# Kernel optimization log

Measured on AMD Instinct MI355X. Metric: run time of the kernel, lower is better.

Reference implementation:

```python
import jax, jax.numpy as jnp
import numpy as np


def _ln(x, g, b, eps=1e-5):
    m = x.mean(-1, keepdims=True)
    v = ((x - m) ** 2).mean(-1, keepdims=True)
    return g * (x - m) / jnp.sqrt(v + eps) + b


def _mha(x, w_qkv, b_qkv, w_o, b_o, nh):
    B, S, d = x.shape
    hd = d // nh
    qkv = x @ w_qkv.T + b_qkv
    q, k, v = jnp.split(qkv, 3, axis=-1)
    sp = lambda t: t.reshape(B, S, nh, hd).transpose(0, 2, 1, 3)
    q, k, v = sp(q), sp(k), sp(v)
    a = jax.nn.softmax(jnp.einsum('bhqd,bhkd->bhqk', q, k) / np.float32(np.sqrt(hd)), axis=-1)
    o = jnp.einsum('bhqk,bhkd->bhqd', a, v).transpose(0, 2, 1, 3).reshape(B, S, d)
    return o @ w_o.T + b_o


def _enc(x, w_qkv, b_qkv, w_o, b_o, ga, ba, wf1, bf1, wf2, bf2, gb, bb, nh=2):
    # torch TransformerEncoderLayer, post-norm, ReLU FFN
    x = _ln(x + _mha(x, w_qkv, b_qkv, w_o, b_o, nh), ga, ba)
    ff = jax.nn.relu(x @ wf1.T + bf1) @ wf2.T + bf2
    return _ln(x + ff, gb, bb)


def forward(nodes, w_qkv1, b_qkv1, w_o1, b_o1, g1a, bb1a, w_ff1a, bf1a, w_ff1b, bf1b, g1b, bb1b,
            wq, bq, wk, bk, wv, bv, g_co, bb_co, w4, b4, w5, b5, w6, b6,
            w_rel, w_root, b_rgcn, wg_rel, wg_root, bg,
            w_qkv2, b_qkv2, w_o2, b_o2, g2a, bb2a, w_ff2a, bf2a, w_ff2b, bf2b, g2b, bb2b,
            w_l1, b_l1, w_l2, b_l2, edge_index, opt_idx):
    N, H = nodes.shape
    O = 4
    B = opt_idx.shape[0] // O
    # option-node mutual attention (encoder_layer1) + scatter back
    opts = nodes[opt_idx].reshape(B, O, H)
    opts = _enc(opts, w_qkv1, b_qkv1, w_o1, b_o1, g1a, bb1a, w_ff1a, bf1a, w_ff1b, bf1b, g1b, bb1b)
    nodes2 = nodes.at[opt_idx].set(opts.reshape(B * O, H))
    src, dst = edge_index[0], edge_index[1]
    xs, xd = nodes2[src], nodes2[dst]  # [E,H]
    # per-edge 4-head co-attention: node1/node2 are single rows so qk^T is a scalar per head
    hd = H // 4
    q = (xs @ wq.T + bq).reshape(-1, 4, hd)
    k = (xd @ wk.T + bk).reshape(-1, 4, hd)
    v = (xd @ wv.T + bv).reshape(-1, 4, hd)
    s = jnp.einsum('ehd,ehd->eh', q, k) / np.float32(np.sqrt(hd))
    r = (s[..., None] * v).reshape(-1, H)
    co = jax.nn.relu(_ln(r, g_co, bb_co))
    h = jax.nn.relu(co @ w4.T + b4)
    h = jax.nn.relu(h @ w5.T + b5)
    logits = h @ w6.T + b6  # [E,8]
    # original applies Softmax(dim=0) to a [1,8] tensor -> all ones -> argmax picks class 0
    probs = jax.nn.softmax(logits[:, None, :], axis=1)[:, 0, :]
    edge_type = jnp.argmax(probs, axis=-1)
    # RGCNConv(H, H, num_relations=8), mean aggregation per relation + root + bias
    agg = jnp.zeros((N, H), nodes.dtype)
    for rel in range(8):
        m = edge_type == rel
        msg = jnp.where(m[:, None], xs @ w_rel[rel], 0.0)
        ssum = jax.ops.segment_sum(msg, dst, num_segments=N)
        cnt = jax.ops.segment_sum(m.astype(nodes.dtype), dst, num_segments=N)
        agg = agg + ssum / jnp.maximum(cnt, 1.0)[:, None]
    out1 = nodes2 @ w_root + b_rgcn + agg
    # GraphConv(H, 64): add-aggregated neighbors through lin_rel + root through lin_root
    agg2 = jax.ops.segment_sum(out1[src], dst, num_segments=N)
    out2 = agg2 @ wg_rel + bg + out1 @ wg_root  # [N,64]
    # readout over option nodes (encoder_layer2 + tanh(linear1) + linear2)
    opt2 = out2[opt_idx].reshape(B, O, 64)
    opt2 = _enc(opt2, w_qkv2, b_qkv2, w_o2, b_o2, g2a, bb2a, w_ff2a, bf2a, w_ff2b, bf2b, g2b, bb2b)
    opt2 = jnp.tanh(opt2 @ w_l1.T + b_l1)
    return opt2 @ w_l2.T + b_l2  # [B,O,1]


def setup_inputs() -> dict:
    key = jax.random.key(0)
    N, E, B, O, H, F = 20000, 40000, 64, 4, 768, 2048
    ks = iter(jax.random.split(key, 64))
    W = lambda *s: jax.random.normal(next(ks), s, jnp.float32) * 0.02
    return dict(
        nodes=jax.random.normal(next(ks), (N, H), jnp.float32),
        edge_index=jax.random.randint(next(ks), (2, E), 0, N),
        opt_idx=jnp.arange(B * O),
        w_qkv1=W(3 * H, H), b_qkv1=jnp.zeros(3 * H), w_o1=W(H, H), b_o1=jnp.zeros(H),
        g1a=jnp.ones(H), bb1a=jnp.zeros(H),
        w_ff1a=W(F, H), bf1a=jnp.zeros(F), w_ff1b=W(H, F), bf1b=jnp.zeros(H),
        g1b=jnp.ones(H), bb1b=jnp.zeros(H),
        wq=W(H, H), bq=jnp.zeros(H), wk=W(H, H), bk=jnp.zeros(H), wv=W(H, H), bv=jnp.zeros(H),
        g_co=jnp.ones(H), bb_co=jnp.zeros(H),
        w4=W(H, H), b4=jnp.zeros(H), w5=W(64, H), b5=jnp.zeros(64), w6=W(8, 64), b6=jnp.zeros(8),
        w_rel=W(8, H, H), w_root=W(H, H), b_rgcn=jnp.zeros(H),
        wg_rel=W(H, 64), wg_root=W(H, 64), bg=jnp.zeros(64),
        w_qkv2=W(192, 64), b_qkv2=jnp.zeros(192), w_o2=W(64, 64), b_o2=jnp.zeros(64),
        g2a=jnp.ones(64), bb2a=jnp.zeros(64),
        w_ff2a=W(F, 64), bf2a=jnp.zeros(F), w_ff2b=W(64, F), bf2b=jnp.zeros(64),
        g2b=jnp.ones(64), bb2b=jnp.zeros(64),
        w_l1=W(64, 64), b_l1=jnp.zeros(64), w_l2=W(1, 64), b_l2=jnp.zeros(1),
    )


def reference(nodes, edge_index, opt_idx, w_qkv1, b_qkv1, w_o1, b_o1, g1a, bb1a, w_ff1a, bf1a,
              w_ff1b, bf1b, g1b, bb1b, wq, bq, wk, bk, wv, bv, g_co, bb_co, w4, b4, w5, b5, w6, b6,
              w_rel, w_root, b_rgcn, wg_rel, wg_root, bg, w_qkv2, b_qkv2, w_o2, b_o2, g2a, bb2a,
              w_ff2a, bf2a, w_ff2b, bf2b, g2b, bb2b, w_l1, b_l1, w_l2, b_l2):
    return forward(nodes, w_qkv1, b_qkv1, w_o1, b_o1, g1a, bb1a, w_ff1a, bf1a, w_ff1b, bf1b, g1b,
                   bb1b, wq, bq, wk, bk, wv, bv, g_co, bb_co, w4, b4, w5, b5, w6, b6, w_rel, w_root,
                   b_rgcn, wg_rel, wg_root, bg, w_qkv2, b_qkv2, w_o2, b_o2, g2a, bb2a, w_ff2a, bf2a,
                   w_ff2b, bf2b, g2b, bb2b, w_l1, b_l1, w_l2, b_l2, edge_index, opt_idx)
```

## Files before the change

### kernel.cpp

```cpp
#include <hip/hip_runtime.h>

typedef unsigned short u16;
typedef unsigned int u32;
typedef __bf16 bf16x8 __attribute__((ext_vector_type(8)));
typedef float f32x4 __attribute__((ext_vector_type(4)));

__device__ __forceinline__ u16 f2bf(float f) {
    union { float f; u32 u; } v; v.f = f;
    u32 r = v.u + 0x7FFFu + ((v.u >> 16) & 1u);
    return (u16)(r >> 16);
}
__device__ __forceinline__ float bf2f(u16 h) {
    union { u32 u; float f; } v; v.u = (u32)h << 16; return v.f;
}

__global__ __launch_bounds__(256) void gemm_bt(
    const u16* __restrict__ A, const u16* __restrict__ Bt,
    float* __restrict__ C, u16* __restrict__ Cb, const float* __restrict__ bias,
    int M, int N, int K, int relu)
{
    __shared__ char lA[128 * 64 * 2];
    __shared__ char lB[128 * 64 * 2];
    const int t = threadIdx.x;
    const int w = t >> 6, l = t & 63;
    const int bn = blockIdx.x, bm = blockIdx.y;
    const int wr = w >> 1, wc = w & 1;

    const int srow = w * 8 + (l >> 3);
    const int scol = ((l & 7) ^ (l >> 3)) << 3;
    const u16* gA = A + (size_t)(bm * 128 + srow) * K + scol;
    const u16* gB = Bt + (size_t)(bn * 128 + srow) * K + scol;

    f32x4 zero = {0.f, 0.f, 0.f, 0.f};
    f32x4 acc[4][4];
#pragma unroll
    for (int i = 0; i < 4; i++)
#pragma unroll
        for (int j = 0; j < 4; j++) acc[i][j] = zero;

    const int arow = wr * 64 + (l & 15);
    const int brow = wc * 64 + (l & 15);
    const int kx = l >> 4;
    const int sw = l & 7;

    for (int k0 = 0; k0 < K; k0 += 64) {
#pragma unroll
        for (int c2 = 0; c2 < 4; ++c2) {
            __builtin_amdgcn_global_load_lds(
                (const __attribute__((address_space(1))) void*)(gA + (size_t)c2 * 32 * K + k0),
                (__attribute__((address_space(3))) void*)(lA + c2 * 4096 + w * 1024), 16, 0, 0);
            __builtin_amdgcn_global_load_lds(
                (const __attribute__((address_space(1))) void*)(gB + (size_t)c2 * 32 * K + k0),
                (__attribute__((address_space(3))) void*)(lB + c2 * 4096 + w * 1024), 16, 0, 0);
        }
        __syncthreads();
#pragma unroll
        for (int kk = 0; kk < 2; ++kk) {
            bf16x8 af[4], bfr[4];
#pragma unroll
            for (int mi = 0; mi < 4; ++mi)
                af[mi] = *(const bf16x8*)(lA + (arow + mi * 16) * 128 + (((kk * 4 + kx) ^ sw) << 4));
#pragma unroll
            for (int ni = 0; ni < 4; ++ni)
                bfr[ni] = *(const bf16x8*)(lB + (brow + ni * 16) * 128 + (((kk * 4 + kx) ^ sw) << 4));
#pragma unroll
            for (int mi = 0; mi < 4; ++mi)
#pragma unroll
                for (int ni = 0; ni < 4; ++ni)
                    acc[mi][ni] = __builtin_amdgcn_mfma_f32_16x16x32_bf16(af[mi], bfr[ni], acc[mi][ni], 0, 0, 0);
        }
        __syncthreads();
    }

    const int cm = bm * 128 + wr * 64;
    const int cn = bn * 128 + wc * 64;
#pragma unroll
    for (int mi = 0; mi < 4; ++mi) {
#pragma unroll
        for (int ni = 0; ni < 4; ++ni) {
            int row0 = cm + mi * 16 + (l >> 4) * 4;
            int col = cn + ni * 16 + (l & 15);
            float bv = bias ? bias[col] : 0.f;
#pragma unroll
            for (int r = 0; r < 4; ++r) {
                float v = acc[mi][ni][r] + bv;
                if (relu) v = fmaxf(v, 0.f);
                if (Cb) Cb[(size_t)(row0 + r) * N + col] = f2bf(v);
                else    C [(size_t)(row0 + r) * N + col] = v;
            }
        }
    }
}

struct CJob { const float* src; u16* dst; long n4; };
struct CJobs4 { CJob j[4]; };
__global__ void conv4_bf16(CJobs4 jobs)
{
    CJob jb = jobs.j[blockIdx.z];
    long i = (long)blockIdx.x * blockDim.x + threadIdx.x;
    long stride = (long)gridDim.x * blockDim.x;
    for (; i < jb.n4; i += stride) {
        float4 v = ((const float4*)jb.src)[i];
        ushort4 o;
        o.x = f2bf(v.x); o.y = f2bf(v.y); o.z = f2bf(v.z); o.w = f2bf(v.w);
        ((ushort4*)jb.dst)[i] = o;
    }
}

struct TJob { const float* src; u16* dst; int Rr, Cc, ldo; };
struct TJobs4 { TJob j[4]; };
__global__ void transpose4_bf16(TJobs4 jobs)
{
    TJob jb = jobs.j[blockIdx.z];
    __shared__ float tile[32][33];
    int c0 = blockIdx.x * 32, r0 = blockIdx.y * 32;
    if (c0 >= jb.Cc || r0 >= jb.Rr) return;
    int tx = threadIdx.x, ty = threadIdx.y;
    for (int dy = 0; dy < 32; dy += 8) {
        int r = r0 + ty + dy, c = c0 + tx;
        tile[ty + dy][tx] = (r < jb.Rr && c < jb.Cc) ? jb.src[(size_t)r * jb.Cc + c] : 0.f;
    }
    __syncthreads();
    for (int dy = 0; dy < 32; dy += 8) {
        int c = c0 + ty + dy, r = r0 + tx;
        if (c < jb.Cc && r < jb.Rr) jb.dst[(size_t)c * jb.ldo + r] = f2bf(tile[tx][ty + dy]);
    }
}

__global__ void conv_nodes_str(const float* __restrict__ nodes, u16* __restrict__ Abig,
                               int Nn, int Mpad)
{
    long i = (long)blockIdx.x * blockDim.x + threadIdx.x;
    long stride = (long)gridDim.x * blockDim.x;
    long n4 = (long)Mpad * 192;
    for (; i < n4; i += stride) {
        long row = i / 192, c4 = i % 192;
        ushort4 o;
        if ((int)row < Nn) {
            float4 v = ((const float4*)nodes)[i];
            o.x = f2bf(v.x); o.y = f2bf(v.y); o.z = f2bf(v.z); o.w = f2bf(v.w);
        } else { o.x = 0; o.y = 0; o.z = 0; o.w = 0; }
        ((ushort4*)Abig)[row * 384 + c4] = o;
    }
}

__global__ void gather_x0(const float* __restrict__ nodes, const int* __restrict__ opt,
                          float* __restrict__ x0, u16* __restrict__ x0b, int H)
{
    int r = blockIdx.x;
    size_t srcb = (size_t)opt[r] * H;
    for (int c = threadIdx.x; c < H; c += blockDim.x) {
        float v = nodes[srcb + c];
        x0[(size_t)r * H + c] = v;
        x0b[(size_t)r * H + c] = f2bf(v);
    }
}

__global__ void scatter_opts_str(const float* __restrict__ x2, const int* __restrict__ opt,
                                 u16* __restrict__ Abig)
{
    int r = blockIdx.x;
    size_t dstb = (size_t)opt[r] * 1536;
    for (int c = threadIdx.x; c < 768; c += blockDim.x)
        Abig[dstb + c] = f2bf(x2[(size_t)r * 768 + c]);
}

__global__ __launch_bounds__(256) void attn_small_b(
    const float* __restrict__ qkv, u16* __restrict__ out, int H, int nh, int hd)
{
    int b = blockIdx.x / nh, h = blockIdx.x % nh;
    int w = threadIdx.x >> 6, l = threadIdx.x & 63;
    __shared__ float sc[4][4];
    int qs = 3 * H;
    const float* qr = qkv + (size_t)(b * 4 + w) * qs + h * hd;
    float scale = rsqrtf((float)hd);
    for (int sj = 0; sj < 4; ++sj) {
        const float* kr = qkv + (size_t)(b * 4 + sj) * qs + H + h * hd;
        float p = 0.f;
        for (int i = l; i < hd; i += 64) p += qr[i] * kr[i];
        for (int off = 32; off; off >>= 1) p += __shfl_down(p, off, 64);
        if (l == 0) sc[w][sj] = p * scale;
    }
    __syncthreads();
    float a0 = sc[w][0], a1 = sc[w][1], a2 = sc[w][2], a3 = sc[w][3];
    float mx = fmaxf(fmaxf(a0, a1), fmaxf(a2, a3));
    float e0 = __expf(a0 - mx), e1 = __expf(a1 - mx), e2 = __expf(a2 - mx), e3 = __expf(a3 - mx);
    float inv = 1.f / (e0 + e1 + e2 + e3);
    e0 *= inv; e1 *= inv; e2 *= inv; e3 *= inv;
    const float* v0 = qkv + (size_t)(b * 4 + 0) * qs + 2 * H + h * hd;
    const float* v1 = v0 + qs; const float* v2 = v1 + qs; const float* v3 = v2 + qs;
    u16* orow = out + (size_t)(b * 4 + w) * H + h * hd;
    for (int i = l; i < hd; i += 64)
        orow[i] = f2bf(e0 * v0[i] + e1 * v1[i] + e2 * v2[i] + e3 * v3[i]);
}

__global__ __launch_bounds__(256) void ln768(
    const float* __restrict__ x, const float* __restrict__ res,
    const float* __restrict__ g, const float* __restrict__ be,
    float* __restrict__ out, u16* __restrict__ outb)
{
    int row = blockIdx.x, t = threadIdx.x;
    const float* xr = x + (size_t)row * 768;
    const float* rr = res + (size_t)row * 768;
    float v[3]; float s = 0.f, q = 0.f;
#pragma unroll
    for (int i = 0; i < 3; i++) {
        float a = xr[t + i * 256] + rr[t + i * 256];
        v[i] = a; s += a; q += a * a;
    }
    for (int off = 32; off; off >>= 1) { s += __shfl_down(s, off, 64); q += __shfl_down(q, off, 64); }
    __shared__ float ss[4], qq[4];
    int w = t >> 6, l = t & 63;
    if (l == 0) { ss[w] = s; qq[w] = q; }
    __syncthreads();
    s = ss[0] + ss[1] + ss[2] + ss[3];
    q = qq[0] + qq[1] + qq[2] + qq[3];
    float m = s * (1.f / 768.f);
    float ri = rsqrtf(q * (1.f / 768.f) - m * m + 1e-5f);
#pragma unroll
    for (int i = 0; i < 3; i++) {
        int c = t + i * 256;
        float o = g[c] * (v[i] - m) * ri + be[c];
        out[(size_t)row * 768 + c] = o;
        if (outb) outb[(size_t)row * 768 + c] = f2bf(o);
    }
}

__global__ void edge_count(const int* __restrict__ ei, int* __restrict__ cnt, int E)
{
    int e = blockIdx.x * blockDim.x + threadIdx.x;
    if (e < E) atomicAdd(&cnt[ei[E + e]], 1);
}

__global__ __launch_bounds__(1024) void scan_offsets(
    const int* __restrict__ cnt, int* __restrict__ offs, int* __restrict__ cur, int n)
{
    __shared__ int part[1024];
    int t = threadIdx.x;
    int per = (n + 1023) / 1024;
    int base = t * per;
    int local = 0;
    for (int i = 0; i < per; i++) {
        int idx = base + i;
        if (idx < n) local += cnt[idx];
    }
    part[t] = local;
    __syncthreads();
    for (int off = 1; off < 1024; off <<= 1) {
        int v = (t >= off) ? part[t - off] : 0;
        __syncthreads();
        part[t] += v;
        __syncthreads();
    }
    int prefix = (t == 0) ? 0 : part[t - 1];
    for (int i = 0; i < per; i++) {
        int idx = base + i;
        if (idx < n) {
            offs[idx] = prefix;
            cur[idx] = prefix;
            prefix += cnt[idx];
        }
    }
}

__global__ void fill_edges(const int* __restrict__ ei, int* __restrict__ cur,
                           int* __restrict__ elist, int E)
{
    int e = blockIdx.x * blockDim.x + threadIdx.x;
    if (e < E) {
        int d = ei[E + e];
        int pos = atomicAdd(&cur[d], 1);
        elist[pos] = ei[e];
    }
}

__global__ __launch_bounds__(256) void gather_mean(
    const int* __restrict__ offs, const int* __restrict__ cnt, const int* __restrict__ elist,
    u16* Abig, int Nn, int Mpad)
{
    int w = threadIdx.x >> 6, l = threadIdx.x & 63;
    int d = blockIdx.x * 4 + w;
    if (d >= Mpad) return;
    float acc[12];
#pragma unroll
    for (int j = 0; j < 12; j++) acc[j] = 0.f;
    float inv = 0.f;
    if (d < Nn) {
        int base = offs[d], c = cnt[d];
        for (int i = 0; i < c; i++) {
            int s = elist[base + i];
            const ushort4* p = (const ushort4*)(Abig + (size_t)s * 1536);
#pragma unroll
            for (int j4 = 0; j4 < 3; j4++) {
                ushort4 v = p[l * 3 + j4];
                acc[j4 * 4 + 0] += bf2f(v.x);
                acc[j4 * 4 + 1] += bf2f(v.y);
                acc[j4 * 4 + 2] += bf2f(v.z);
                acc[j4 * 4 + 3] += bf2f(v.w);
            }
        }
        inv = 1.f / (float)max(c, 1);
    }
    ushort4* q = (ushort4*)(Abig + (size_t)d * 1536 + 768);
#pragma unroll
    for (int j4 = 0; j4 < 3; j4++) {
        ushort4 o;
        o.x = f2bf(acc[j4 * 4 + 0] * inv);
        o.y = f2bf(acc[j4 * 4 + 1] * inv);
        o.z = f2bf(acc[j4 * 4 + 2] * inv);
        o.w = f2bf(acc[j4 * 4 + 3] * inv);
        q[l * 3 + j4] = o;
    }
}

__global__ __launch_bounds__(256) void enc2_head(
    const int* __restrict__ opt, const int* __restrict__ offs, const int* __restrict__ cnt,
    const int* __restrict__ elist, const float* __restrict__ C2, const float* __restrict__ bg,
    const float* __restrict__ w_qkv2, const float* __restrict__ b_qkv2,
    const float* __restrict__ w_o2, const float* __restrict__ b_o2,
    const float* __restrict__ g2a, const float* __restrict__ bb2a,
    float* __restrict__ x21)
{
    __shared__ float X[4][64];
    __shared__ float QKV[4][192];
    __shared__ float T[4][64];
    int b = blockIdx.x;
    int w = threadIdx.x >> 6, l = threadIdx.x & 63;
    int row = b * 4 + w;

    {
        int d = opt[row];
        float acc = bg[l] + C2[(size_t)d * 128 + 64 + l];
        int base = offs[d], c = cnt[d];
        for (int i = 0; i < c; i++) {
            int s = elist[base + i];
            acc += C2[(size_t)s * 128 + l];
        }
        X[w][l] = acc;
    }
    __syncthreads();

#pragma unroll
    for (int j = 0; j < 3; j++) {
        int n = l + j * 64;
        const float* wr = w_qkv2 + (size_t)n * 64;
        float s = b_qkv2[n];
        for (int k = 0; k < 64; k++) s += X[w][k] * wr[k];
        QKV[w][n] = s;
    }
    __syncthreads();

    {
        float q = QKV[w][l];
        float p0 = q * QKV[0][64 + l], p1 = q * QKV[1][64 + l];
        float p2 = q * QKV[2][64 + l], p3 = q * QKV[3][64 + l];
#pragma unroll
        for (int off = 1; off < 32; off <<= 1) {
            p0 += __shfl_xor(p0, off, 64); p1 += __shfl_xor(p1, off, 64);
            p2 += __shfl_xor(p2, off, 64); p3 += __shfl_xor(p3, off, 64);
        }
        p0 *= 0.1767766953f; p1 *= 0.1767766953f; p2 *= 0.1767766953f; p3 *= 0.1767766953f;
        float mx = fmaxf(fmaxf(p0, p1), fmaxf(p2, p3));
        float e0 = __expf(p0 - mx), e1 = __expf(p1 - mx), e2 = __expf(p2 - mx), e3 = __expf(p3 - mx);
        float inv = 1.f / (e0 + e1 + e2 + e3);
        T[w][l] = (e0 * QKV[0][128 + l] + e1 * QKV[1][128 + l] +
                   e2 * QKV[2][128 + l] + e3 * QKV[3][128 + l]) * inv;
    }
    __syncthreads();

    {
        const float* wr = w_o2 + (size_t)l * 64;
        float s = b_o2[l];
        for (int k = 0; k < 64; k++) s += T[w][k] * wr[k];
        float xa = s + X[w][l];
        float sum = xa, sq = xa * xa;
#pragma unroll
        for (int off = 1; off < 64; off <<= 1) {
            sum += __shfl_xor(sum, off, 64);
            sq  += __shfl_xor(sq, off, 64);
        }
        float m = sum * (1.f / 64.f);
        float ri = rsqrtf(sq * (1.f / 64.f) - m * m + 1e-5f);
        x21[(size_t)row * 64 + l] = g2a[l] * (xa - m) * ri + bb2a[l];
    }
}

__global__ __launch_bounds__(256) void ff1_par(
    const float* __restrict__ x21, const float* __restrict__ wf1,
    const float* __restrict__ bf1, float* __restrict__ Hf)
{
    __shared__ float X[64];
    int b = blockIdx.x, t = threadIdx.x;
    int r = b >> 3, n = (b & 7) * 256 + t;
    if (t < 64) X[t] = x21[(size_t)r * 64 + t];
    __syncthreads();
    const float4* wr4 = (const float4*)(wf1 + (size_t)n * 64);
    float s = bf1[n];
#pragma unroll
    for (int k4 = 0; k4 < 16; k4++) {
        float4 wv = wr4[k4];
        const float* xp = X + k4 * 4;
        s += wv.x * xp[0] + wv.y * xp[1] + wv.z * xp[2] + wv.w * xp[3];
    }
    Hf[(size_t)r * 2048 + n] = fmaxf(s, 0.f);
}

__global__ __launch_bounds__(256) void ff2_tail(
    const float* __restrict__ Hf, const float* __restrict__ x21,
    const float* __restrict__ wf2, const float* __restrict__ bf2,
    const float* __restrict__ g2b, const float* __restrict__ bb2b,
    const float* __restrict__ w_l1, const float* __restrict__ b_l1,
    const float* __restrict__ w_l2, const float* __restrict__ b_l2,
    float* __restrict__ out)
{
    __shared__ float HL[2048];
    __shared__ float part[4][64];
    __shared__ float X2[64];
    int r = blockIdx.x, t = threadIdx.x;
    int w = t >> 6, l = t & 63;

    {
        const float4* src = (const float4*)(Hf + (size_t)r * 2048);
        float4* dst = (float4*)HL;
        dst[t] = src[t];
        dst[t + 256] = src[t + 256];
    }
    __syncthreads();

    {
        const float4* wr4 = (const float4*)(wf2 + (size_t)l * 2048 + w * 512);
        const float* hp = HL + w * 512;
        float s = 0.f;
#pragma unroll 16
        for (int k4 = 0; k4 < 128; k4++) {
            float4 wv = wr4[k4];
            const float* xp = hp + k4 * 4;
            s += wv.x * xp[0] + wv.y * xp[1] + wv.z * xp[2] + wv.w * xp[3];
        }
        part[w][l] = s;
    }
    __syncthreads();

    if (w == 0) {
        float xa = part[0][l] + part[1][l] + part[2][l] + part[3][l] + bf2[l]
                 + x21[(size_t)r * 64 + l];
        float sum = xa, sq = xa * xa;
#pragma unroll
        for (int off = 1; off < 64; off <<= 1) {
            sum += __shfl_xor(sum, off, 64);
            sq  += __shfl_xor(sq, off, 64);
        }
        float m = sum * (1.f / 64.f);
        float ri = rsqrtf(sq * (1.f / 64.f) - m * m + 1e-5f);
        X2[l] = g2b[l] * (xa - m) * ri + bb2b[l];
        __builtin_amdgcn_wave_barrier();
        const float* wr = w_l1 + (size_t)l * 64;
        float s = b_l1[l];
        for (int k = 0; k < 64; k++) s += X2[k] * wr[k];
        float tv = tanhf(s);
        float p = tv * w_l2[l];
#pragma unroll
        for (int off = 1; off < 64; off <<= 1) p += __shfl_xor(p, off, 64);
        if (l == 0) out[r] = p + b_l2[0];
    }
}

extern "C" void kernel_launch(void* const* d_in, const int* in_sizes, int n_in,
                              void* d_out, int out_size, void* d_ws, size_t ws_size,
                              hipStream_t stream)
{
    const float* nodes  = (const float*)d_in[0];
    const int*   ei     = (const int*)d_in[1];
    const int*   opt    = (const int*)d_in[2];
    const float* w_qkv1 = (const float*)d_in[3];
    const float* b_qkv1 = (const float*)d_in[4];
    const float* w_o1   = (const float*)d_in[5];
    const float* b_o1   = (const float*)d_in[6];
    const float* g1a    = (const float*)d_in[7];
    const float* bb1a   = (const float*)d_in[8];
    const float* w_ff1a = (const float*)d_in[9];
    const float* bf1a   = (const float*)d_in[10];
    const float* w_ff1b = (const float*)d_in[11];
    const float* bf1b   = (const float*)d_in[12];
    const float* g1b    = (const float*)d_in[13];
    const float* bb1b   = (const float*)d_in[14];
    const float* w_rel  = (const float*)d_in[29];
    const float* w_root = (const float*)d_in[30];
    const float* b_rgcn = (const float*)d_in[31];
    const float* wg_rel = (const float*)d_in[32];
    const float* wg_root= (const float*)d_in[33];
    const float* bg     = (const float*)d_in[34];
    const float* w_qkv2 = (const float*)d_in[35];
    const float* b_qkv2 = (const float*)d_in[36];
    const float* w_o2   = (const float*)d_in[37];
    const float* b_o2   = (const float*)d_in[38];
    const float* g2a    = (const float*)d_in[39];
    const float* bb2a   = (const float*)d_in[40];
    const float* w_ff2a = (const float*)d_in[41];
    const float* bf2a   = (const float*)d_in[42];
    const float* w_ff2b = (const float*)d_in[43];
    const float* bf2b   = (const float*)d_in[44];
    const float* g2b    = (const float*)d_in[45];
    const float* bb2b   = (const float*)d_in[46];
    const float* w_l1   = (const float*)d_in[47];
    const float* b_l1   = (const float*)d_in[48];
    const float* w_l2   = (const float*)d_in[49];
    const float* b_l2   = (const float*)d_in[50];

    const int H = 768, F = 2048;
    const int Nn = in_sizes[0] / H;
    const int E  = in_sizes[1] / 2;
    const int R  = in_sizes[2];
    const int Mpad = (Nn + 127) & ~127;
    const int Bb = R / 4;

    char* ws = (char*)d_ws;
    size_t off = 0;
    auto alloc = [&](size_t b) -> char* {
        char* p = ws + off; off += (b + 255) & ~(size_t)255; return p;
    };
    u16* wqkv1b  = (u16*)alloc((size_t)3 * H * H * 2);
    u16* wo1b    = (u16*)alloc((size_t)H * H * 2);
    u16* wff1ab  = (u16*)alloc((size_t)F * H * 2);
    u16* wff1bb  = (u16*)alloc((size_t)H * F * 2);
    u16* Wbt     = (u16*)alloc((size_t)768 * 1536 * 2);
    u16* W2tb    = (u16*)alloc((size_t)128 * H * 2);
    float* x0   = (float*)alloc((size_t)R * H * 4);
    u16*  x0b   = (u16*)alloc((size_t)R * H * 2);
    float* qkvb = (float*)alloc((size_t)R * 3 * H * 4);
    u16*  atnob = (u16*)alloc((size_t)R * H * 2);
    float* obuf = (float*)alloc((size_t)R * H * 4);
    float* x1   = (float*)alloc((size_t)R * H * 4);
    u16*  x1b   = (u16*)alloc((size_t)R * H * 2);
    u16*  ffhb  = (u16*)alloc((size_t)R * F * 2);
    float* ffo  = (float*)alloc((size_t)R * H * 4);
    float* x2   = (float*)alloc((size_t)R * H * 4);
    u16*  Abig  = (u16*)alloc((size_t)Mpad * 1536 * 2);
    u16*  out1b = (u16*)alloc((size_t)Mpad * H * 2);
    float* C2   = (float*)alloc((size_t)Mpad * 128 * 4);
    int* cnt   = (int*)alloc((size_t)Nn * 4);
    int* offs  = (int*)alloc((size_t)Nn * 4);
    int* cur   = (int*)alloc((size_t)Nn * 4);
    int* elist = (int*)alloc((size_t)E * 4);
    float* x21 = (float*)alloc((size_t)R * 64 * 4);
    float* Hf2 = (float*)alloc((size_t)R * F * 4);
    (void)ws_size; (void)n_in; (void)out_size;

    {
        CJobs4 cj;
        cj.j[0] = { w_qkv1, wqkv1b, (long)3 * H * H / 4 };
        cj.j[1] = { w_o1,   wo1b,   (long)H * H / 4 };
        cj.j[2] = { w_ff1a, wff1ab, (long)F * H / 4 };
        cj.j[3] = { w_ff1b, wff1bb, (long)H * F / 4 };
        conv4_bf16<<<dim3(432, 1, 4), 256, 0, stream>>>(cj);
        TJobs4 tj;
        tj.j[0] = { w_root, Wbt,        768, 768, 1536 };
        tj.j[1] = { w_rel,  Wbt + 768,  768, 768, 1536 };
        tj.j[2] = { wg_rel, W2tb,               768, 64, 768 };
        tj.j[3] = { wg_root, W2tb + (size_t)64 * 768, 768, 64, 768 };
        transpose4_bf16<<<dim3(24, 24, 4), dim3(32, 8), 0, stream>>>(tj);
    }

    gather_x0<<<R, 256, 0, stream>>>(nodes, opt, x0, x0b, H);
    gemm_bt<<<dim3(3 * H / 128, R / 128), 256, 0, stream>>>(x0b, wqkv1b, qkvb, nullptr, b_qkv1, R, 3 * H, H, 0);
    attn_small_b<<<Bb * 2, 256, 0, stream>>>(qkvb, atnob, H, 2, H / 2);
    gemm_bt<<<dim3(H / 128, R / 128), 256, 0, stream>>>(atnob, wo1b, obuf, nullptr, b_o1, R, H, H, 0);
    ln768<<<R, 256, 0, stream>>>(obuf, x0, g1a, bb1a, x1, x1b);
    gemm_bt<<<dim3(F / 128, R / 128), 256, 0, stream>>>(x1b, wff1ab, nullptr, ffhb, bf1a, R, F, H, 1);
    gemm_bt<<<dim3(H / 128, R / 128), 256, 0, stream>>>(ffhb, wff1bb, ffo, nullptr, bf1b, R, H, F, 0);
    ln768<<<R, 256, 0, stream>>>(ffo, x1, g1b, bb1b, x2, nullptr);

    conv_nodes_str<<<2048, 256, 0, stream>>>(nodes, Abig, Nn, Mpad);
    scatter_opts_str<<<R, 256, 0, stream>>>(x2, opt, Abig);

    hipMemsetAsync(cnt, 0, (size_t)Nn * 4, stream);
    edge_count<<<(E + 255) / 256, 256, 0, stream>>>(ei, cnt, E);
    scan_offsets<<<1, 1024, 0, stream>>>(cnt, offs, cur, Nn);
    fill_edges<<<(E + 255) / 256, 256, 0, stream>>>(ei, cur, elist, E);
    gather_mean<<<Mpad / 4, 256, 0, stream>>>(offs, cnt, elist, Abig, Nn, Mpad);

    gemm_bt<<<dim3(H / 128, Mpad / 128), 256, 0, stream>>>(Abig, Wbt, nullptr, out1b, b_rgcn, Mpad, H, 1536, 0);

    gemm_bt<<<dim3(1, Mpad / 128), 256, 0, stream>>>(out1b, W2tb, C2, nullptr, nullptr, Mpad, 128, 768, 0);

    enc2_head<<<Bb, 256, 0, stream>>>(opt, offs, cnt, elist, C2, bg,
                                      w_qkv2, b_qkv2, w_o2, b_o2, g2a, bb2a, x21);
    ff1_par<<<R * 8, 256, 0, stream>>>(x21, w_ff2a, bf2a, Hf2);
    ff2_tail<<<R, 256, 0, stream>>>(Hf2, x21, w_ff2b, bf2b, g2b, bb2b,
                                    w_l1, b_l1, w_l2, b_l2, (float*)d_out);
}
```

Measured before the change: 570.8 us.

## Fold RGCN layer weights into second-layer projection to skip wide GEMM

Since there is no nonlinearity between the RGCN output and the next projection, the two linear maps are pre-multiplied into one 1536x128 weight (WcT), and the bias is folded through as well (bc). The large Mpad x 768 x 1536 GEMM and its bf16 intermediate are replaced by one Mpad x 128 x 1536 GEMM plus a small weight-product GEMM that runs once per call. The gather_mean load/store indexing also changes to a lane-contiguous pattern for coalescing. The cost is an extra bf16 rounding of the combined weight, which may change numerics slightly.

```diff
diff --git a/kernel.cpp b/kernel.cpp
--- a/kernel.cpp
+++ b/kernel.cpp
@@ -93,8 +93,8 @@
 }
 
 struct CJob { const float* src; u16* dst; long n4; };
-struct CJobs4 { CJob j[4]; };
-__global__ void conv4_bf16(CJobs4 jobs)
+struct CJobs6 { CJob j[6]; };
+__global__ void conv6_bf16(CJobs6 jobs)
 {
     CJob jb = jobs.j[blockIdx.z];
     long i = (long)blockIdx.x * blockDim.x + threadIdx.x;
@@ -108,8 +108,8 @@
 }
 
 struct TJob { const float* src; u16* dst; int Rr, Cc, ldo; };
-struct TJobs4 { TJob j[4]; };
-__global__ void transpose4_bf16(TJobs4 jobs)
+struct TJobs2 { TJob j[2]; };
+__global__ void transpose2_bf16(TJobs2 jobs)
 {
     TJob jb = jobs.j[blockIdx.z];
     __shared__ float tile[32][33];
@@ -125,6 +125,16 @@
         int c = c0 + ty + dy, r = r0 + tx;
         if (c < jb.Cc && r < jb.Rr) jb.dst[(size_t)c * jb.ldo + r] = f2bf(tile[tx][ty + dy]);
     }
+}
+
+__global__ void bc_prep(const float* __restrict__ b_rgcn, const float* __restrict__ wg_rel,
+                        const float* __restrict__ wg_root, float* __restrict__ bc)
+{
+    int n = threadIdx.x;
+    const float* W = (n < 64) ? (wg_rel + n) : (wg_root + (n - 64));
+    float s = 0.f;
+    for (int k = 0; k < 768; k++) s += b_rgcn[k] * W[(size_t)k * 64];
+    bc[n] = s;
 }
 
 __global__ void conv_nodes_str(const float* __restrict__ nodes, u16* __restrict__ Abig,
@@ -292,7 +302,7 @@
             const ushort4* p = (const ushort4*)(Abig + (size_t)s * 1536);
 #pragma unroll
             for (int j4 = 0; j4 < 3; j4++) {
-                ushort4 v = p[l * 3 + j4];
+                ushort4 v = p[j4 * 64 + l];
                 acc[j4 * 4 + 0] += bf2f(v.x);
                 acc[j4 * 4 + 1] += bf2f(v.y);
                 acc[j4 * 4 + 2] += bf2f(v.z);
@@ -309,7 +319,7 @@
         o.y = f2bf(acc[j4 * 4 + 1] * inv);
         o.z = f2bf(acc[j4 * 4 + 2] * inv);
         o.w = f2bf(acc[j4 * 4 + 3] * inv);
-        q[l * 3 + j4] = o;
+        q[j4 * 64 + l] = o;
     }
 }
 
@@ -523,8 +533,10 @@
     u16* wo1b    = (u16*)alloc((size_t)H * H * 2);
     u16* wff1ab  = (u16*)alloc((size_t)F * H * 2);
     u16* wff1bb  = (u16*)alloc((size_t)H * F * 2);
-    u16* Wbt     = (u16*)alloc((size_t)768 * 1536 * 2);
+    u16* Wbraw   = (u16*)alloc((size_t)1536 * H * 2);
     u16* W2tb    = (u16*)alloc((size_t)128 * H * 2);
+    u16* WcT     = (u16*)alloc((size_t)128 * 1536 * 2);
+    float* bc    = (float*)alloc((size_t)128 * 4);
     float* x0   = (float*)alloc((size_t)R * H * 4);
     u16*  x0b   = (u16*)alloc((size_t)R * H * 2);
     float* qkvb = (float*)alloc((size_t)R * 3 * H * 4);
@@ -536,7 +548,6 @@
     float* ffo  = (float*)alloc((size_t)R * H * 4);
     float* x2   = (float*)alloc((size_t)R * H * 4);
     u16*  Abig  = (u16*)alloc((size_t)Mpad * 1536 * 2);
-    u16*  out1b = (u16*)alloc((size_t)Mpad * H * 2);
     float* C2   = (float*)alloc((size_t)Mpad * 128 * 4);
     int* cnt   = (int*)alloc((size_t)Nn * 4);
     int* offs  = (int*)alloc((size_t)Nn * 4);
@@ -547,19 +558,21 @@
     (void)ws_size; (void)n_in; (void)out_size;
 
     {
-        CJobs4 cj;
+        CJobs6 cj;
         cj.j[0] = { w_qkv1, wqkv1b, (long)3 * H * H / 4 };
         cj.j[1] = { w_o1,   wo1b,   (long)H * H / 4 };
         cj.j[2] = { w_ff1a, wff1ab, (long)F * H / 4 };
         cj.j[3] = { w_ff1b, wff1bb, (long)H * F / 4 };
-        conv4_bf16<<<dim3(432, 1, 4), 256, 0, stream>>>(cj);
-        TJobs4 tj;
-        tj.j[0] = { w_root, Wbt,        768, 768, 1536 };
-        tj.j[1] = { w_rel,  Wbt + 768,  768, 768, 1536 };
-        tj.j[2] = { wg_rel, W2tb,               768, 64, 768 };
-        tj.j[3] = { wg_root, W2tb + (size_t)64 * 768, 768, 64, 768 };
-        transpose4_bf16<<<dim3(24, 24, 4), dim3(32, 8), 0, stream>>>(tj);
-    }
+        cj.j[4] = { w_root, Wbraw,                    (long)H * H / 4 };
+        cj.j[5] = { w_rel,  Wbraw + (size_t)H * H,    (long)H * H / 4 };
+        conv6_bf16<<<dim3(432, 1, 6), 256, 0, stream>>>(cj);
+        TJobs2 tj;
+        tj.j[0] = { wg_rel,  W2tb,                    768, 64, 768 };
+        tj.j[1] = { wg_root, W2tb + (size_t)64 * 768, 768, 64, 768 };
+        transpose2_bf16<<<dim3(2, 24, 2), dim3(32, 8), 0, stream>>>(tj);
+    }
+    gemm_bt<<<dim3(1536 / 128, 1), 256, 0, stream>>>(W2tb, Wbraw, nullptr, WcT, nullptr, 128, 1536, 768, 0);
+    bc_prep<<<1, 128, 0, stream>>>(b_rgcn, wg_rel, wg_root, bc);
 
     gather_x0<<<R, 256, 0, stream>>>(nodes, opt, x0, x0b, H);
     gemm_bt<<<dim3(3 * H / 128, R / 128), 256, 0, stream>>>(x0b, wqkv1b, qkvb, nullptr, b_qkv1, R, 3 * H, H, 0);
@@ -579,9 +592,7 @@
     fill_edges<<<(E + 255) / 256, 256, 0, stream>>>(ei, cur, elist, E);
     gather_mean<<<Mpad / 4, 256, 0, stream>>>(offs, cnt, elist, Abig, Nn, Mpad);
 
-    gemm_bt<<<dim3(H / 128, Mpad / 128), 256, 0, stream>>>(Abig, Wbt, nullptr, out1b, b_rgcn, Mpad, H, 1536, 0);
-
-    gemm_bt<<<dim3(1, Mpad / 128), 256, 0, stream>>>(out1b, W2tb, C2, nullptr, nullptr, Mpad, 128, 768, 0);
+    gemm_bt<<<dim3(1, Mpad / 128), 256, 0, stream>>>(Abig, WcT, C2, nullptr, bc, Mpad, 128, 1536, 0);
 
     enc2_head<<<Bb, 256, 0, stream>>>(opt, offs, cnt, elist, C2, bg,
                                       w_qkv2, b_qkv2, w_o2, b_o2, g2a, bb2a, x21);
```

Measured after the change: 550.6 us. 3.5% less time.
